# Optimization experiments

Measured on AMD Instinct MI355X. Metric: run time of the kernel, lower is better.

Reference implementation:

```python
import jax, jax.numpy as jnp
import numpy as np
from jax import lax

B, CIN, IMG = 32, 3, 128   # batch, image channels, image size
D, K = 256, 512            # codebook dim, codebook size


def _conv(x, w, stride, pad):
    # PyTorch Conv2d (bias=False), NCHW / OIHW
    return lax.conv_general_dilated(x, w, (stride, stride), ((pad, pad), (pad, pad)),
                                    dimension_numbers=('NCHW', 'OIHW', 'NCHW'))


def _deconv(x, w, b):
    # PyTorch ConvTranspose2d(k=4, s=2, p=1): lhs_dilation=2, pad=k-1-p=2, flipped kernel,
    # weight layout (in, out, kh, kw) -> 'IOHW'
    y = lax.conv_general_dilated(x, jnp.flip(w, (2, 3)), (1, 1), ((2, 2), (2, 2)),
                                 lhs_dilation=(2, 2),
                                 dimension_numbers=('NCHW', 'IOHW', 'NCHW'))
    return y + b[None, :, None, None]


def _res(x, w1, w2):
    # Faithful to the source ResidualBlock: relu1 output is DISCARDED (conv1 applied to x)
    out = _conv(x, w1, 1, 1)      # 3x3, pad 1
    out = jax.nn.relu(out)
    out = _conv(out, w2, 1, 0)    # 1x1, pad 0
    return out + x


def setup_inputs() -> dict:
    key = jax.random.key(0)
    ks = jax.random.split(key, 20)
    s = 0.05
    inp = {
        'x': jax.random.uniform(ks[0], (B, CIN, IMG, IMG), jnp.float32),
        # codebook, init uniform(-1/K, 1/K) as in init_weights
        'embed_w': jax.random.uniform(ks[1], (K, D), jnp.float32, -1.0 / K, 1.0 / K),
        # encoder
        'e_w1': jax.random.normal(ks[2], (D, CIN, 4, 4), jnp.float32) * s,
        'e_w2': jax.random.normal(ks[3], (D, D, 4, 4), jnp.float32) * s,
        'e_r1a': jax.random.normal(ks[4], (D, D, 3, 3), jnp.float32) * s,
        'e_r1b': jax.random.normal(ks[5], (D, D, 1, 1), jnp.float32) * s,
        'e_r2a': jax.random.normal(ks[6], (D, D, 3, 3), jnp.float32) * s,
        'e_r2b': jax.random.normal(ks[7], (D, D, 1, 1), jnp.float32) * s,
        # decoder
        'd_r1a': jax.random.normal(ks[8], (D, D, 3, 3), jnp.float32) * s,
        'd_r1b': jax.random.normal(ks[9], (D, D, 1, 1), jnp.float32) * s,
        'd_r2a': jax.random.normal(ks[10], (D, D, 3, 3), jnp.float32) * s,
        'd_r2b': jax.random.normal(ks[11], (D, D, 1, 1), jnp.float32) * s,
        'dt1_w': jax.random.normal(ks[12], (D, D, 4, 4), jnp.float32) * s,  # (in,out,kh,kw)
        'dt1_b': jnp.zeros((D,), jnp.float32),
        'dt2_w': jax.random.normal(ks[13], (D, CIN, 4, 4), jnp.float32) * s,
        'dt2_b': jnp.zeros((CIN,), jnp.float32),
    }
    return inp


def reference(x, embed_w, e_w1, e_w2, e_r1a, e_r1b, e_r2a, e_r2b,
              d_r1a, d_r1b, d_r2a, d_r2b, dt1_w, dt1_b, dt2_w, dt2_b):
    # ---- encoder (BN layers exist but are never called in the source forward) ----
    h = jax.nn.relu(_conv(x, e_w1, 2, 1))          # (B,D,64,64)
    h = jax.nn.relu(_conv(h, e_w2, 2, 1))          # (B,D,32,32)
    h = _res(h, e_r1a, e_r1b)
    z_e = _res(h, e_r2a, e_r2b)                    # (B,D,H,W)

    # ---- vector quantisation ----
    ze = jnp.transpose(z_e, (0, 2, 3, 1))          # (B,H,W,D)
    # squared L2 distances via expansion (same argmin/values as the broadcast diff tensor)
    d2 = (jnp.sum(ze * ze, -1, keepdims=True)      # (B,H,W,1)
          - 2.0 * jnp.einsum('bhwd,kd->bhwk', ze, embed_w)
          + jnp.sum(embed_w * embed_w, -1))        # (B,H,W,K)
    dist = jnp.sqrt(jnp.maximum(d2, 0.0))          # torch.norm(p=2) before min
    idx = jnp.argmin(dist, axis=-1)                # (B,H,W)
    z_q = embed_w[idx]                             # (B,H,W,D) gather

    # losses: source averages over an extra duplicated K axis, identical to mean over B,H,W
    sg = lax.stop_gradient
    loss1 = jnp.mean(jnp.sum((ze - sg(z_q)) ** 2, -1))   # grads -> encoder
    loss2 = jnp.mean(jnp.sum((sg(ze) - z_q) ** 2, -1))   # grads -> codebook

    # ---- decoder (takes z_q; BN layers never called; relu after deconv1 only) ----
    dq = jnp.transpose(z_q, (0, 3, 1, 2))          # (B,D,H,W)
    dq = _res(dq, d_r1a, d_r1b)
    dq = _res(dq, d_r2a, d_r2b)
    dq = jax.nn.relu(_deconv(dq, dt1_w, dt1_b))    # (B,D,64,64)
    recon = jax.nn.sigmoid(_deconv(dq, dt2_w, dt2_b))  # (B,3,128,128)
    return recon, loss1, loss2
```

## Files before the change

### kernel.cpp

```cpp
#include <hip/hip_runtime.h>


typedef __attribute__((ext_vector_type(8))) short bf16x8;
typedef __attribute__((ext_vector_type(4))) float f32x4;
#define MFMA_B16(a, b, c) __builtin_amdgcn_mfma_f32_16x16x32_bf16(a, b, c, 0, 0, 0)

__device__ inline unsigned short f2b(float f) {
    unsigned int u = __float_as_uint(f);
    unsigned int r = u + 0x7fffu + ((u >> 16) & 1u);
    return (unsigned short)(r >> 16);
}
__device__ inline float b2f(unsigned short u) {
    return __uint_as_float(((unsigned int)u) << 16);
}

struct PermfArgs {
    const float* src[10];
    int kw[10];
    int so[10], si[10], sh[10], sw[10];
    int cum[11];
};

__global__ void prep_all_k(PermfArgs a, unsigned short* __restrict__ dst,
                           const float* __restrict__ dt2_w, unsigned short* __restrict__ wg,
                           const float* __restrict__ embed, unsigned short* __restrict__ embF,
                           const float* __restrict__ e_w1, unsigned short* __restrict__ wgc,
                           float* __restrict__ nrm, float* __restrict__ lacc)
{
    int blkid = blockIdx.x;
    int tid = threadIdx.x;
    if (blkid < 18432) {
        int gid = blkid * 256 + tid;
        if (gid >= a.cum[10]) return;
        int seg = 0;
        while (seg < 9 && gid >= a.cum[seg + 1]) ++seg;
        int l = gid - a.cum[seg];
        int q = l & 31;
        int n = (l >> 5) & 255;
        int rest = l >> 13;
        int cch = rest & 7;
        int khkw = rest >> 3;
        int kh = khkw / a.kw[seg], kw = khkw % a.kw[seg];
        int ci = cch * 32 + q;
        dst[gid] = f2b(a.src[seg][n * a.so[seg] + ci * a.si[seg] + kh * a.sh[seg] + kw * a.sw[seg]]);
        return;
    }
    int blk = blkid - 18432;
    if (blk < 48) {
        int idx = blk * 256 + tid;
        int q = idx & 31;
        int n = (idx >> 5) % 48;
        int cch = idx / (48 * 32);
        int ci = cch * 32 + q;
        int oc = n % 3, khkw = n / 3;
        int kh = khkw >> 2, kw = khkw & 3;
        wg[idx] = f2b(dt2_w[ci * 48 + oc * 16 + kh * 4 + kw]);
    } else if (blk < 560) {
        int idx = (blk - 48) * 256 + tid;
        int q = idx & 31;
        int n = (idx >> 5) & 511;
        int cch = idx >> 14;
        embF[idx] = f2b(embed[n * 256 + cch * 32 + q]);
    } else if (blk < 624) {
        int idx = (blk - 560) * 256 + tid;
        int q = idx & 31;
        int n = (idx >> 5) & 255;
        int kt = idx >> 13;
        int k = kt * 32 + q;
        float v = 0.f;
        if (k < 48) {
            int ci = k >> 4, kh = (k >> 2) & 3, kwv = k & 3;
            v = e_w1[n * 48 + ci * 16 + kh * 4 + kwv];
        }
        wgc[idx] = f2b(v);
    } else if (blk < 752) {
        int row = (blk - 624) * 4 + (tid >> 6);
        int lane = tid & 63;
        float s = 0.f;
        #pragma unroll
        for (int c = 0; c < 256; c += 64) {
            float v = embed[row * 256 + c + lane];
            s += v * v;
        }
        #pragma unroll
        for (int off = 1; off < 64; off <<= 1) s += __shfl_xor(s, off);
        if (lane == 0) nrm[row] = s;
    } else {
        if (tid == 0) lacc[0] = 0.f;
    }
}

__global__ void __launch_bounds__(256, 4)
conv1m_k(const float* __restrict__ x, const unsigned short* __restrict__ wgc,
         unsigned short* __restrict__ out)
{
    int bh = blockIdx.x;
    int b = bh >> 6, oh = bh & 63;
    int tid = threadIdx.x;
    int lane = tid & 63, wv = tid >> 6;
    int m = lane & 15, quad = lane >> 4;
    __shared__ float xrow[3][4][130];
    __shared__ __align__(16) unsigned short imc[64 * 72];
    __shared__ __align__(16) unsigned short obuf[32 * 264];
    for (int s = tid; s < 1560; s += 256) {
        int col = s % 130;
        int t = s / 130;
        int r = t & 3;
        int c = t >> 2;
        int ih = 2 * oh - 1 + r, iw = col - 1;
        float v = 0.f;
        if ((unsigned)ih < 128u && (unsigned)iw < 128u)
            v = x[(((b * 3 + c) << 7) + ih) * 128 + iw];
        xrow[c][r][col] = v;
    }
    __syncthreads();
    for (int s = tid; s < 4096; s += 256) {
        int px = s >> 6, k = s & 63;
        float v = 0.f;
        if (k < 48) {
            int ci = k >> 4, kh = (k >> 2) & 3, kw = k & 3;
            v = xrow[ci][kh][2 * px + kw];
        }
        imc[px * 72 + k] = f2b(v);
    }
    __syncthreads();
    f32x4 acc[16];
    f32x4 z = {0.f, 0.f, 0.f, 0.f};
    #pragma unroll
    for (int i = 0; i < 16; ++i) acc[i] = z;
    bf16x8 a0 = *(const bf16x8*)&imc[((wv << 4) + m) * 72 + (quad << 3)];
    bf16x8 a1 = *(const bf16x8*)&imc[((wv << 4) + m) * 72 + 32 + (quad << 3)];
    #pragma unroll
    for (int nt = 0; nt < 16; ++nt) {
        bf16x8 b0 = *(const bf16x8*)&wgc[(nt * 16 + m) * 32 + (quad << 3)];
        bf16x8 b1 = *(const bf16x8*)&wgc[(256 + nt * 16 + m) * 32 + (quad << 3)];
        acc[nt] = MFMA_B16(a0, b0, acc[nt]);
        acc[nt] = MFMA_B16(a1, b1, acc[nt]);
    }
    for (int h = 0; h < 2; ++h) {
        __syncthreads();
        if ((wv >> 1) == h) {
            #pragma unroll
            for (int nt = 0; nt < 16; ++nt)
                #pragma unroll
                for (int r = 0; r < 4; ++r) {
                    int pxl = ((wv & 1) << 4) + quad * 4 + r;
                    obuf[pxl * 264 + nt * 16 + m] = f2b(fmaxf(acc[nt][r], 0.f));
                }
        }
        __syncthreads();
        int pxl2 = tid >> 3, seg = tid & 7;
        int gp = (bh << 6) + 32 * h + pxl2;
        #pragma unroll
        for (int u = 0; u < 4; ++u)
            *(int4*)&out[(gp << 8) + seg * 32 + u * 8] = *(int4*)&obuf[pxl2 * 264 + seg * 32 + u * 8];
    }
}

__global__ void __launch_bounds__(256, 4)
mconv2_k(const unsigned short* __restrict__ in, const unsigned short* __restrict__ wf,
         unsigned short* __restrict__ out)
{
    int blk = blockIdx.x;
    int bb = blk >> 5;
    int rem = blk & 31;
    int j = rem >> 1;
    int nh = rem & 1;
    int tid = threadIdx.x;
    int lane = tid & 63;
    int wv = tid >> 6;
    int n0 = (nh << 7) + (wv << 5);
    int m = lane & 15, quad = lane >> 4;
    __shared__ __align__(16) unsigned short win[2 * 66 * 132];
    f32x4 acc[2][2][2];
    f32x4 z = {0.f, 0.f, 0.f, 0.f};
    #pragma unroll
    for (int a = 0; a < 2; ++a)
        #pragma unroll
        for (int i = 0; i < 2; ++i)
            #pragma unroll
            for (int t = 0; t < 2; ++t) acc[a][i][t] = z;

    for (int c0 = 0; c0 < 256; c0 += 128) {
        for (int kh = 0; kh < 4; ++kh) {
            __syncthreads();
            for (int s = tid; s < 2 * 66 * 16; s += 256) {
                int c16 = s & 15;
                int t2 = s >> 4;
                int col = t2 % 66;
                int rr = t2 / 66;
                int ih = 4 * j - 1 + kh + 2 * rr, iw = col - 1;
                int4 v = make_int4(0, 0, 0, 0);
                if ((unsigned)ih < 64u && (unsigned)iw < 64u)
                    v = *(const int4*)&in[((((bb << 6) + ih) << 6) + iw) * 256 + c0 + (c16 << 3)];
                int cs = (col >> 1) + (col & 1) * 33;
                *(int4*)&win[(rr * 66 + cs) * 132 + (c16 << 3)] = v;
            }
            __syncthreads();
            #pragma unroll
            for (int kw = 0; kw < 4; ++kw) {
                int csoff = (kw >> 1) + (kw & 1) * 33;
                #pragma unroll
                for (int cch = 0; cch < 4; ++cch) {
                    bf16x8 a00 = *(const bf16x8*)&win[(m + csoff) * 132 + (cch << 5) + (quad << 3)];
                    bf16x8 a01 = *(const bf16x8*)&win[(m + 16 + csoff) * 132 + (cch << 5) + (quad << 3)];
                    bf16x8 a10 = *(const bf16x8*)&win[(66 + m + csoff) * 132 + (cch << 5) + (quad << 3)];
                    bf16x8 a11 = *(const bf16x8*)&win[(66 + m + 16 + csoff) * 132 + (cch << 5) + (quad << 3)];
                    int cg = (c0 >> 5) + cch;
                    int wbase = ((((kh << 2) + kw) * 8 + cg) * 256 + n0 + m) * 32 + (quad << 3);
                    bf16x8 b0 = *(const bf16x8*)&wf[wbase];
                    bf16x8 b1 = *(const bf16x8*)&wf[wbase + 16 * 32];
                    acc[0][0][0] = MFMA_B16(a00, b0, acc[0][0][0]);
                    acc[0][0][1] = MFMA_B16(a00, b1, acc[0][0][1]);
                    acc[0][1][0] = MFMA_B16(a01, b0, acc[0][1][0]);
                    acc[0][1][1] = MFMA_B16(a01, b1, acc[0][1][1]);
                    acc[1][0][0] = MFMA_B16(a10, b0, acc[1][0][0]);
                    acc[1][0][1] = MFMA_B16(a10, b1, acc[1][0][1]);
                    acc[1][1][0] = MFMA_B16(a11, b0, acc[1][1][0]);
                    acc[1][1][1] = MFMA_B16(a11, b1, acc[1][1][1]);
                }
            }
        }
    }
    for (int row = 0; row < 2; ++row) {
        __syncthreads();
        #pragma unroll
        for (int mt = 0; mt < 2; ++mt)
            #pragma unroll
            for (int nt = 0; nt < 2; ++nt)
                #pragma unroll
                for (int r = 0; r < 4; ++r) {
                    int px = mt * 16 + quad * 4 + r;
                    int lcol = (wv << 5) + nt * 16 + m;
                    win[px * 136 + lcol] = f2b(fmaxf(acc[row][mt][nt][r], 0.f));
                }
        __syncthreads();
        int oh = 2 * j + row;
        int px2 = tid >> 3, seg = tid & 7;
        int gb = ((((bb << 5) + oh) << 5) + px2) * 256 + (nh << 7) + seg * 16;
        *(int4*)&out[gb]     = *(int4*)&win[px2 * 136 + seg * 16];
        *(int4*)&out[gb + 8] = *(int4*)&win[px2 * 136 + seg * 16 + 8];
    }
}

__global__ void __launch_bounds__(256, 4)
mres_k(const unsigned short* __restrict__ in, const unsigned short* __restrict__ wf3,
       const unsigned short* __restrict__ wf1, const unsigned short* __restrict__ res,
       unsigned short* __restrict__ outb, float* __restrict__ outf, int f32out)
{
    int blk = blockIdx.x;
    int bb = blk >> 5, oh = blk & 31;
    int tid = threadIdx.x;
    int lane = tid & 63;
    int n0 = (tid >> 6) << 6;
    int m = lane & 15, quad = lane >> 4;
    __shared__ __align__(16) unsigned short win[3 * 34 * 132];
    f32x4 acc[2][4];
    f32x4 z = {0.f, 0.f, 0.f, 0.f};
    #pragma unroll
    for (int i = 0; i < 2; ++i)
        #pragma unroll
        for (int t = 0; t < 4; ++t) acc[i][t] = z;

    for (int c0 = 0; c0 < 256; c0 += 128) {
        __syncthreads();
        for (int s = tid; s < 3 * 34 * 16; s += 256) {
            int c16 = s & 15;
            int t2 = s >> 4;
            int col = t2 % 34;
            int rr = t2 / 34;
            int ih = oh - 1 + rr, iw = col - 1;
            int4 v = make_int4(0, 0, 0, 0);
            if ((unsigned)ih < 32u && (unsigned)iw < 32u)
                v = *(const int4*)&in[((((bb << 5) + ih) << 5) + iw) * 256 + c0 + (c16 << 3)];
            *(int4*)&win[(rr * 34 + col) * 132 + (c16 << 3)] = v;
        }
        __syncthreads();
        for (int kh = 0; kh < 3; ++kh) {
            #pragma unroll
            for (int kw = 0; kw < 3; ++kw) {
                #pragma unroll
                for (int cch = 0; cch < 4; ++cch) {
                    const unsigned short* ba = &win[(kh * 34 + m + kw) * 132 + (cch << 5) + (quad << 3)];
                    bf16x8 a0 = *(const bf16x8*)ba;
                    bf16x8 a1 = *(const bf16x8*)(ba + 16 * 132);
                    int cg = (c0 >> 5) + cch;
                    int wbase = (((kh * 3 + kw) * 8 + cg) * 256 + n0 + m) * 32 + (quad << 3);
                    bf16x8 b0 = *(const bf16x8*)&wf3[wbase];
                    bf16x8 b1 = *(const bf16x8*)&wf3[wbase + 16 * 32];
                    bf16x8 b2 = *(const bf16x8*)&wf3[wbase + 32 * 32];
                    bf16x8 b3 = *(const bf16x8*)&wf3[wbase + 48 * 32];
                    acc[0][0] = MFMA_B16(a0, b0, acc[0][0]);
                    acc[0][1] = MFMA_B16(a0, b1, acc[0][1]);
                    acc[0][2] = MFMA_B16(a0, b2, acc[0][2]);
                    acc[0][3] = MFMA_B16(a0, b3, acc[0][3]);
                    acc[1][0] = MFMA_B16(a1, b0, acc[1][0]);
                    acc[1][1] = MFMA_B16(a1, b1, acc[1][1]);
                    acc[1][2] = MFMA_B16(a1, b2, acc[1][2]);
                    acc[1][3] = MFMA_B16(a1, b3, acc[1][3]);
                }
            }
        }
    }

    __syncthreads();
    unsigned short* mid = win;
    #pragma unroll
    for (int mt = 0; mt < 2; ++mt)
        #pragma unroll
        for (int nt = 0; nt < 4; ++nt)
            #pragma unroll
            for (int r = 0; r < 4; ++r) {
                int px = mt * 16 + quad * 4 + r;
                int col = n0 + nt * 16 + m;
                mid[px * 264 + col] = f2b(fmaxf(acc[mt][nt][r], 0.f));
            }
    __syncthreads();

    f32x4 acc2[2][4];
    #pragma unroll
    for (int i = 0; i < 2; ++i)
        #pragma unroll
        for (int t = 0; t < 4; ++t) acc2[i][t] = z;
    #pragma unroll
    for (int cch = 0; cch < 8; ++cch) {
        bf16x8 a0 = *(const bf16x8*)&mid[m * 264 + (cch << 5) + (quad << 3)];
        bf16x8 a1 = *(const bf16x8*)&mid[(m + 16) * 264 + (cch << 5) + (quad << 3)];
        int wbase = (cch * 256 + n0 + m) * 32 + (quad << 3);
        bf16x8 b0 = *(const bf16x8*)&wf1[wbase];
        bf16x8 b1 = *(const bf16x8*)&wf1[wbase + 16 * 32];
        bf16x8 b2 = *(const bf16x8*)&wf1[wbase + 32 * 32];
        bf16x8 b3 = *(const bf16x8*)&wf1[wbase + 48 * 32];
        acc2[0][0] = MFMA_B16(a0, b0, acc2[0][0]);
        acc2[0][1] = MFMA_B16(a0, b1, acc2[0][1]);
        acc2[0][2] = MFMA_B16(a0, b2, acc2[0][2]);
        acc2[0][3] = MFMA_B16(a0, b3, acc2[0][3]);
        acc2[1][0] = MFMA_B16(a1, b0, acc2[1][0]);
        acc2[1][1] = MFMA_B16(a1, b1, acc2[1][1]);
        acc2[1][2] = MFMA_B16(a1, b2, acc2[1][2]);
        acc2[1][3] = MFMA_B16(a1, b3, acc2[1][3]);
    }
    __syncthreads();
    #pragma unroll
    for (int mt = 0; mt < 2; ++mt)
        #pragma unroll
        for (int nt = 0; nt < 4; ++nt)
            #pragma unroll
            for (int r = 0; r < 4; ++r) {
                int px = mt * 16 + quad * 4 + r;
                int col = n0 + nt * 16 + m;
                mid[px * 264 + col] = f2b(acc2[mt][nt][r]);
            }
    __syncthreads();
    int rowbase = blk << 13;
    int px2 = tid >> 3, seg = tid & 7;
    #pragma unroll
    for (int u = 0; u < 4; ++u) {
        int c0 = seg * 32 + u * 8;
        int gb = rowbase + (px2 << 8) + c0;
        int4 av4 = *(const int4*)&mid[px2 * 264 + c0];
        int4 rv4 = *(const int4*)&res[gb];
        const unsigned short* ap = (const unsigned short*)&av4;
        const unsigned short* rp = (const unsigned short*)&rv4;
        float v[8];
        unsigned short ob[8];
        #pragma unroll
        for (int j2 = 0; j2 < 8; ++j2) {
            v[j2] = b2f(ap[j2]) + b2f(rp[j2]);
            ob[j2] = f2b(v[j2]);
        }
        *(int4*)&outb[gb] = *(int4*)ob;
        if (f32out) {
            *(float4*)&outf[gb] = make_float4(v[0], v[1], v[2], v[3]);
            *(float4*)&outf[gb + 4] = make_float4(v[4], v[5], v[6], v[7]);
        }
    }
}

__global__ void __launch_bounds__(256, 4)
mdeconv1_k(const unsigned short* __restrict__ in, const unsigned short* __restrict__ wf,
           const float* __restrict__ bias, unsigned short* __restrict__ out)
{
    int blk = blockIdx.x;
    int bb = blk >> 5;
    int rem = blk & 31;
    int pp = rem >> 4;
    int i = rem & 15;
    int oy_a = pp + 4 * i;
    int p = (oy_a + 1) & 1;
    int r0a = (oy_a + 1 - p) >> 1;
    int rbase = r0a - 1;
    int tid = threadIdx.x;
    int lane = tid & 63;
    int n0 = (tid >> 6) << 6;
    int m = lane & 15, quad = lane >> 4;
    __shared__ __align__(16) unsigned short win[3 * 34 * 132];

    for (int par = 0; par < 2; ++par) {
        f32x4 acc[2][2][4];
        f32x4 z = {0.f, 0.f, 0.f, 0.f};
        #pragma unroll
        for (int a = 0; a < 2; ++a)
            #pragma unroll
            for (int i2 = 0; i2 < 2; ++i2)
                #pragma unroll
                for (int t = 0; t < 4; ++t) acc[a][i2][t] = z;

        for (int c0 = 0; c0 < 256; c0 += 128) {
            __syncthreads();
            for (int s = tid; s < 3 * 34 * 16; s += 256) {
                int c16 = s & 15;
                int t2 = s >> 4;
                int col = t2 % 34;
                int rr = t2 / 34;
                int ih = rbase + rr, iw = col - 1;
                int4 v = make_int4(0, 0, 0, 0);
                if ((unsigned)ih < 32u && (unsigned)iw < 32u)
                    v = *(const int4*)&in[((((bb << 5) + ih) << 5) + iw) * 256 + c0 + (c16 << 3)];
                *(int4*)&win[(rr * 34 + col) * 132 + (c16 << 3)] = v;
            }
            __syncthreads();
            #pragma unroll
            for (int t = 0; t < 2; ++t) {
                int kh = p + 2 * t;
                #pragma unroll
                for (int u = 0; u < 2; ++u) {
                    int kw = (1 - par) + 2 * u;
                    int ixoff = par - u + 1;
                    #pragma unroll
                    for (int cch = 0; cch < 4; ++cch) {
                        const unsigned short* baA = &win[((1 - t) * 34 + m + ixoff) * 132 + (cch << 5) + (quad << 3)];
                        const unsigned short* baB = &win[((2 - t) * 34 + m + ixoff) * 132 + (cch << 5) + (quad << 3)];
                        bf16x8 a00 = *(const bf16x8*)baA;
                        bf16x8 a01 = *(const bf16x8*)(baA + 16 * 132);
                        bf16x8 a10 = *(const bf16x8*)baB;
                        bf16x8 a11 = *(const bf16x8*)(baB + 16 * 132);
                        int cg = (c0 >> 5) + cch;
                        int wbase = ((((kh << 2) + kw) * 8 + cg) * 256 + n0 + m) * 32 + (quad << 3);
                        bf16x8 b0 = *(const bf16x8*)&wf[wbase];
                        bf16x8 b1 = *(const bf16x8*)&wf[wbase + 16 * 32];
                        bf16x8 b2 = *(const bf16x8*)&wf[wbase + 32 * 32];
                        bf16x8 b3 = *(const bf16x8*)&wf[wbase + 48 * 32];
                        acc[0][0][0] = MFMA_B16(a00, b0, acc[0][0][0]);
                        acc[0][0][1] = MFMA_B16(a00, b1, acc[0][0][1]);
                        acc[0][0][2] = MFMA_B16(a00, b2, acc[0][0][2]);
                        acc[0][0][3] = MFMA_B16(a00, b3, acc[0][0][3]);
                        acc[0][1][0] = MFMA_B16(a01, b0, acc[0][1][0]);
                        acc[0][1][1] = MFMA_B16(a01, b1, acc[0][1][1]);
                        acc[0][1][2] = MFMA_B16(a01, b2, acc[0][1][2]);
                        acc[0][1][3] = MFMA_B16(a01, b3, acc[0][1][3]);
                        acc[1][0][0] = MFMA_B16(a10, b0, acc[1][0][0]);
                        acc[1][0][1] = MFMA_B16(a10, b1, acc[1][0][1]);
                        acc[1][0][2] = MFMA_B16(a10, b2, acc[1][0][2]);
                        acc[1][0][3] = MFMA_B16(a10, b3, acc[1][0][3]);
                        acc[1][1][0] = MFMA_B16(a11, b0, acc[1][1][0]);
                        acc[1][1][1] = MFMA_B16(a11, b1, acc[1][1][1]);
                        acc[1][1][2] = MFMA_B16(a11, b2, acc[1][1][2]);
                        acc[1][1][3] = MFMA_B16(a11, b3, acc[1][1][3]);
                    }
                }
            }
        }
        #pragma unroll
        for (int row = 0; row < 2; ++row) {
            int oy = oy_a + 2 * row;
            __syncthreads();
            #pragma unroll
            for (int mt = 0; mt < 2; ++mt)
                #pragma unroll
                for (int nt = 0; nt < 4; ++nt) {
                    int col = n0 + nt * 16 + m;
                    float bs = bias[col];
                    #pragma unroll
                    for (int r = 0; r < 4; ++r) {
                        int oxi = mt * 16 + quad * 4 + r;
                        win[oxi * 264 + col] = f2b(fmaxf(acc[row][mt][nt][r] + bs, 0.f));
                    }
                }
            __syncthreads();
            int oxi2 = tid >> 3, seg = tid & 7;
            int gb = ((((bb << 6) + oy) << 6) + 2 * oxi2 + par) * 256 + seg * 32;
            #pragma unroll
            for (int u = 0; u < 4; ++u)
                *(int4*)&out[gb + u * 8] = *(int4*)&win[oxi2 * 264 + seg * 32 + u * 8];
        }
    }
}

__global__ void __launch_bounds__(256, 2)
vqm_k(const unsigned short* __restrict__ zeb, const float* __restrict__ zef,
      const unsigned short* __restrict__ embF, const float* __restrict__ embed,
      const float* __restrict__ nrm, unsigned short* __restrict__ zq,
      float* __restrict__ lacc)
{
    int bh = blockIdx.x;
    int tid = threadIdx.x;
    int lane = tid & 63;
    int wv = tid >> 6;
    int m = lane & 15, quad = lane >> 4;
    __shared__ __align__(16) unsigned short win[32 * 264];
    __shared__ float bvv[4][32];
    __shared__ int   bii[4][32];
    __shared__ int   bidx[32];
    int rowbase = bh << 13;
    for (int s = tid; s < 32 * 32; s += 256) {
        int c8 = s & 31, px = s >> 5;
        *(int4*)&win[px * 264 + (c8 << 3)] = *(const int4*)&zeb[rowbase + (px << 8) + (c8 << 3)];
    }
    __syncthreads();

    f32x4 acc[2][8];
    f32x4 z = {0.f, 0.f, 0.f, 0.f};
    #pragma unroll
    for (int i = 0; i < 2; ++i)
        #pragma unroll
        for (int j = 0; j < 8; ++j) acc[i][j] = z;

    #pragma unroll
    for (int cch = 0; cch < 8; ++cch) {
        bf16x8 a0 = *(const bf16x8*)&win[m * 264 + (cch << 5) + (quad << 3)];
        bf16x8 a1 = *(const bf16x8*)&win[(m + 16) * 264 + (cch << 5) + (quad << 3)];
        #pragma unroll
        for (int nt = 0; nt < 8; ++nt) {
            bf16x8 b = *(const bf16x8*)&embF[((cch << 9) + (wv << 7) + (nt << 4) + m) * 32 + (quad << 3)];
            acc[0][nt] = MFMA_B16(a0, b, acc[0][nt]);
            acc[1][nt] = MFMA_B16(a1, b, acc[1][nt]);
        }
    }

    float nv[8];
    #pragma unroll
    for (int nt = 0; nt < 8; ++nt) nv[nt] = nrm[(wv << 7) + (nt << 4) + m];

    #pragma unroll
    for (int mt = 0; mt < 2; ++mt)
        #pragma unroll
        for (int r = 0; r < 4; ++r) {
            float bv = 1e30f;
            int bi = 0x7fffffff;
            #pragma unroll
            for (int nt = 0; nt < 8; ++nt) {
                float d = nv[nt] - 2.f * acc[mt][nt][r];
                int n = (wv << 7) + (nt << 4) + m;
                if (d < bv || (d == bv && n < bi)) { bv = d; bi = n; }
            }
            #pragma unroll
            for (int off = 1; off < 16; off <<= 1) {
                float ov = __shfl_xor(bv, off);
                int oi = __shfl_xor(bi, off);
                if (ov < bv || (ov == bv && oi < bi)) { bv = ov; bi = oi; }
            }
            if (m == 0) {
                int px = mt * 16 + quad * 4 + r;
                bvv[wv][px] = bv;
                bii[wv][px] = bi;
            }
        }
    __syncthreads();
    if (tid < 32) {
        float bv = bvv[0][tid];
        int bi = bii[0][tid];
        #pragma unroll
        for (int w2 = 1; w2 < 4; ++w2) {
            float ov = bvv[w2][tid];
            int oi = bii[w2][tid];
            if (ov < bv || (ov == bv && oi < bi)) { bv = ov; bi = oi; }
        }
        bidx[tid] = bi;
    }
    __syncthreads();

    float lsum = 0.f;
    #pragma unroll
    for (int j = 0; j < 8; ++j) {
        int px = (wv << 3) + j;
        int bi = bidx[px];
        int pix = (bh << 5) + px;
        const float4 e = *(const float4*)&embed[bi * 256 + (lane << 2)];
        const float4 zv = *(const float4*)&zef[(pix << 8) + (lane << 2)];
        ushort4 eq;
        eq.x = f2b(e.x); eq.y = f2b(e.y); eq.z = f2b(e.z); eq.w = f2b(e.w);
        *(ushort4*)&zq[(pix << 8) + (lane << 2)] = eq;
        float dx = zv.x - e.x, dy = zv.y - e.y, dz = zv.z - e.z, dw = zv.w - e.w;
        lsum += dx * dx + dy * dy + dz * dz + dw * dw;
    }
    #pragma unroll
    for (int off = 1; off < 64; off <<= 1) lsum += __shfl_xor(lsum, off);
    if (lane == 0) atomicAdd(lacc, lsum);
}

__global__ void __launch_bounds__(256, 4)
mdec2a_k(const unsigned short* __restrict__ in, const unsigned short* __restrict__ wg,
         float* __restrict__ Y)
{
    int tid = threadIdx.x;
    int lane = tid & 63;
    int wv = tid >> 6;
    int m = lane & 15, quad = lane >> 4;
    __shared__ __align__(16) unsigned short win[64 * 264];
    int pxbase = blockIdx.x << 6;
    for (int s = tid; s < 64 * 32; s += 256) {
        int c8 = s & 31, px = s >> 5;
        *(int4*)&win[px * 264 + (c8 << 3)] = *(const int4*)&in[((pxbase + px) << 8) + (c8 << 3)];
    }
    __syncthreads();
    f32x4 acc[3];
    f32x4 z = {0.f, 0.f, 0.f, 0.f};
    acc[0] = z; acc[1] = z; acc[2] = z;
    #pragma unroll
    for (int cch = 0; cch < 8; ++cch) {
        bf16x8 a = *(const bf16x8*)&win[((wv << 4) + m) * 264 + (cch << 5) + (quad << 3)];
        #pragma unroll
        for (int nt = 0; nt < 3; ++nt) {
            bf16x8 b = *(const bf16x8*)&wg[(cch * 48 + nt * 16 + m) * 32 + (quad << 3)];
            acc[nt] = MFMA_B16(a, b, acc[nt]);
        }
    }
    #pragma unroll
    for (int nt = 0; nt < 3; ++nt)
        #pragma unroll
        for (int r = 0; r < 4; ++r) {
            int px = pxbase + (wv << 4) + quad * 4 + r;
            Y[px * 48 + nt * 16 + m] = acc[nt][r];
        }
}

__global__ void dec2b_k(const float* __restrict__ Y, const float* __restrict__ bias,
                        const float* __restrict__ lacc, float* __restrict__ out)
{
    if (blockIdx.x == 0 && threadIdx.x == 0) {
        float mloss = lacc[0] * (1.0f / 32768.0f);
        out[1572864] = mloss;
        out[1572865] = mloss;
    }
    int idx = blockIdx.x * 256 + threadIdx.x;
    int b = idx >> 14;
    int rem = idx & 16383;
    int oy = rem >> 7;
    int ox = rem & 127;
    int p = (oy + 1) & 1;
    int q = (ox + 1) & 1;
    float acc0 = bias[0], acc1 = bias[1], acc2 = bias[2];
    #pragma unroll
    for (int t = 0; t < 2; ++t) {
        int kh = p + 2 * t;
        int ih = (oy + 1 - kh) >> 1;
        if ((unsigned)ih >= 64u) continue;
        #pragma unroll
        for (int u = 0; u < 2; ++u) {
            int kw = q + 2 * u;
            int iw = (ox + 1 - kw) >> 1;
            if ((unsigned)iw >= 64u) continue;
            int base = ((((b << 6) + ih) << 6) + iw) * 48 + ((kh << 2) + kw) * 3;
            acc0 += Y[base];
            acc1 += Y[base + 1];
            acc2 += Y[base + 2];
        }
    }
    int obase = (b * 3 << 14) + (oy << 7) + ox;
    out[obase]           = 1.f / (1.f + expf(-acc0));
    out[obase + 16384]   = 1.f / (1.f + expf(-acc1));
    out[obase + 32768]   = 1.f / (1.f + expf(-acc2));
}

extern "C" void kernel_launch(void* const* d_in, const int* in_sizes, int n_in,
                              void* d_out, int out_size, void* d_ws, size_t ws_size,
                              hipStream_t stream)
{
    (void)in_sizes; (void)n_in; (void)out_size; (void)ws_size;
    const float* x      = (const float*)d_in[0];
    const float* embed  = (const float*)d_in[1];
    const float* e_w1   = (const float*)d_in[2];
    const float* e_w2   = (const float*)d_in[3];
    const float* e_r1a  = (const float*)d_in[4];
    const float* e_r1b  = (const float*)d_in[5];
    const float* e_r2a  = (const float*)d_in[6];
    const float* e_r2b  = (const float*)d_in[7];
    const float* d_r1a  = (const float*)d_in[8];
    const float* d_r1b  = (const float*)d_in[9];
    const float* d_r2a  = (const float*)d_in[10];
    const float* d_r2b  = (const float*)d_in[11];
    const float* dt1_w  = (const float*)d_in[12];
    const float* dt1_b  = (const float*)d_in[13];
    const float* dt2_w  = (const float*)d_in[14];
    const float* dt2_b  = (const float*)d_in[15];
    float* outp = (float*)d_out;

    char* base = (char*)d_ws;
    size_t off = 0;
    auto alloc = [&](size_t bytes) { char* p = base + off; off += (bytes + 255) & ~size_t(255); return p; };
    unsigned short* A0b = (unsigned short*)alloc(67108864);
    float*          A1f = (float*)alloc(33554432);
    unsigned short* L0  = (unsigned short*)alloc(16777216);
    unsigned short* L1  = (unsigned short*)alloc(16777216);
    unsigned short* Wf  = (unsigned short*)alloc(9437184);
    unsigned short* Wg  = (unsigned short*)alloc(24576);
    unsigned short* EmbF = (unsigned short*)alloc(262144);
    unsigned short* WgC = (unsigned short*)alloc(32768);
    float* Nrm  = (float*)alloc(2048);
    float* Lacc = (float*)alloc(64);
    float* Y = A1f;

    unsigned short* Wf_ew2  = Wf;
    unsigned short* Wf_er1a = Wf + 1048576;
    unsigned short* Wf_er1b = Wf + 1638400;
    unsigned short* Wf_er2a = Wf + 1703936;
    unsigned short* Wf_er2b = Wf + 2293760;
    unsigned short* Wf_dr1a = Wf + 2359296;
    unsigned short* Wf_dr1b = Wf + 2949120;
    unsigned short* Wf_dr2a = Wf + 3014656;
    unsigned short* Wf_dr2b = Wf + 3604480;
    unsigned short* Wf_dt1  = Wf + 3670016;

    PermfArgs pa;
    const float* srcs[10] = {e_w2, e_r1a, e_r1b, e_r2a, e_r2b, d_r1a, d_r1b, d_r2a, d_r2b, dt1_w};
    int kws[10] = {4, 3, 1, 3, 1, 3, 1, 3, 1, 4};
    int sos[10] = {4096, 2304, 256, 2304, 256, 2304, 256, 2304, 256, 16};
    int sis[10] = {16, 9, 1, 9, 1, 9, 1, 9, 1, 4096};
    int shs[10] = {4, 3, 0, 3, 0, 3, 0, 3, 0, 4};
    int sws[10] = {1, 1, 0, 1, 0, 1, 0, 1, 0, 1};
    int cums[11] = {0, 1048576, 1638400, 1703936, 2293760, 2359296,
                    2949120, 3014656, 3604480, 3670016, 4718592};
    for (int k = 0; k < 10; ++k) {
        pa.src[k] = srcs[k]; pa.kw[k] = kws[k]; pa.so[k] = sos[k];
        pa.si[k] = sis[k]; pa.sh[k] = shs[k]; pa.sw[k] = sws[k];
        pa.cum[k] = cums[k];
    }
    pa.cum[10] = cums[10];

    prep_all_k<<<19185, 256, 0, stream>>>(pa, Wf, dt2_w, Wg, embed, EmbF, e_w1, WgC, Nrm, Lacc);

    conv1m_k<<<32 * 64, 256, 0, stream>>>(x, WgC, A0b);
    mconv2_k<<<32 * 32, 256, 0, stream>>>(A0b, Wf_ew2, L1);
    mres_k<<<32 * 32, 256, 0, stream>>>(L1, Wf_er1a, Wf_er1b, L1, L0, nullptr, 0);
    mres_k<<<32 * 32, 256, 0, stream>>>(L0, Wf_er2a, Wf_er2b, L0, L1, A1f, 1);

    vqm_k<<<32 * 32, 256, 0, stream>>>(L1, A1f, EmbF, embed, Nrm, L1, Lacc);

    mres_k<<<32 * 32, 256, 0, stream>>>(L1, Wf_dr1a, Wf_dr1b, L1, L0, nullptr, 0);
    mres_k<<<32 * 32, 256, 0, stream>>>(L0, Wf_dr2a, Wf_dr2b, L0, L1, nullptr, 0);
    mdeconv1_k<<<32 * 32, 256, 0, stream>>>(L1, Wf_dt1, dt1_b, A0b);
    mdec2a_k<<<2048, 256, 0, stream>>>(A0b, Wg, Y);
    dec2b_k<<<2048, 256, 0, stream>>>(Y, dt2_b, Lacc, outp);
}
```

Baseline: 856.2 us.

## Stage full channel depth in LDS for res and deconv1, one output row per block

The residual conv kernel now loads all 256 input channels of its 3-row window into LDS at once instead of two 128-channel halves, removing a barrier/reload phase. The first deconvolution kernel is restructured so each block computes one output row (both column parities) from a 2-row full-channel window, doubling the grid and writing a contiguous 64-pixel row with coalesced stores. The change trades larger LDS footprints and lower occupancy bounds for fewer synchronisations and simpler staging, and deconv1 loses the previous sharing of weight loads across two output rows.

```diff
diff --git a/kernel.cpp b/kernel.cpp
--- a/kernel.cpp
+++ b/kernel.cpp
@@ -243,7 +243,7 @@
     }
 }
 
-__global__ void __launch_bounds__(256, 4)
+__global__ void __launch_bounds__(256, 2)
 mres_k(const unsigned short* __restrict__ in, const unsigned short* __restrict__ wf3,
        const unsigned short* __restrict__ wf1, const unsigned short* __restrict__ res,
        unsigned short* __restrict__ outb, float* __restrict__ outf, int f32out)
@@ -254,7 +254,7 @@
     int lane = tid & 63;
     int n0 = (tid >> 6) << 6;
     int m = lane & 15, quad = lane >> 4;
-    __shared__ __align__(16) unsigned short win[3 * 34 * 132];
+    __shared__ __align__(16) unsigned short win[3 * 34 * 264];
     f32x4 acc[2][4];
     f32x4 z = {0.f, 0.f, 0.f, 0.f};
     #pragma unroll
@@ -262,43 +262,40 @@
         #pragma unroll
         for (int t = 0; t < 4; ++t) acc[i][t] = z;
 
-    for (int c0 = 0; c0 < 256; c0 += 128) {
-        __syncthreads();
-        for (int s = tid; s < 3 * 34 * 16; s += 256) {
-            int c16 = s & 15;
-            int t2 = s >> 4;
-            int col = t2 % 34;
-            int rr = t2 / 34;
-            int ih = oh - 1 + rr, iw = col - 1;
-            int4 v = make_int4(0, 0, 0, 0);
-            if ((unsigned)ih < 32u && (unsigned)iw < 32u)
-                v = *(const int4*)&in[((((bb << 5) + ih) << 5) + iw) * 256 + c0 + (c16 << 3)];
-            *(int4*)&win[(rr * 34 + col) * 132 + (c16 << 3)] = v;
-        }
-        __syncthreads();
-        for (int kh = 0; kh < 3; ++kh) {
-            #pragma unroll
-            for (int kw = 0; kw < 3; ++kw) {
-                #pragma unroll
-                for (int cch = 0; cch < 4; ++cch) {
-                    const unsigned short* ba = &win[(kh * 34 + m + kw) * 132 + (cch << 5) + (quad << 3)];
-                    bf16x8 a0 = *(const bf16x8*)ba;
-                    bf16x8 a1 = *(const bf16x8*)(ba + 16 * 132);
-                    int cg = (c0 >> 5) + cch;
-                    int wbase = (((kh * 3 + kw) * 8 + cg) * 256 + n0 + m) * 32 + (quad << 3);
-                    bf16x8 b0 = *(const bf16x8*)&wf3[wbase];
-                    bf16x8 b1 = *(const bf16x8*)&wf3[wbase + 16 * 32];
-                    bf16x8 b2 = *(const bf16x8*)&wf3[wbase + 32 * 32];
-                    bf16x8 b3 = *(const bf16x8*)&wf3[wbase + 48 * 32];
-                    acc[0][0] = MFMA_B16(a0, b0, acc[0][0]);
-                    acc[0][1] = MFMA_B16(a0, b1, acc[0][1]);
-                    acc[0][2] = MFMA_B16(a0, b2, acc[0][2]);
-                    acc[0][3] = MFMA_B16(a0, b3, acc[0][3]);
-                    acc[1][0] = MFMA_B16(a1, b0, acc[1][0]);
-                    acc[1][1] = MFMA_B16(a1, b1, acc[1][1]);
-                    acc[1][2] = MFMA_B16(a1, b2, acc[1][2]);
-                    acc[1][3] = MFMA_B16(a1, b3, acc[1][3]);
-                }
+    for (int s = tid; s < 3 * 34 * 32; s += 256) {
+        int c8 = s & 31;
+        int t2 = s >> 5;
+        int col = t2 % 34;
+        int rr = t2 / 34;
+        int ih = oh - 1 + rr, iw = col - 1;
+        int4 v = make_int4(0, 0, 0, 0);
+        if ((unsigned)ih < 32u && (unsigned)iw < 32u)
+            v = *(const int4*)&in[((((bb << 5) + ih) << 5) + iw) * 256 + (c8 << 3)];
+        *(int4*)&win[(rr * 34 + col) * 264 + (c8 << 3)] = v;
+    }
+    __syncthreads();
+
+    for (int kh = 0; kh < 3; ++kh) {
+        #pragma unroll
+        for (int kw = 0; kw < 3; ++kw) {
+            #pragma unroll
+            for (int cch = 0; cch < 8; ++cch) {
+                const unsigned short* ba = &win[(kh * 34 + m + kw) * 264 + (cch << 5) + (quad << 3)];
+                bf16x8 a0 = *(const bf16x8*)ba;
+                bf16x8 a1 = *(const bf16x8*)(ba + 16 * 264);
+                int wbase = (((kh * 3 + kw) * 8 + cch) * 256 + n0 + m) * 32 + (quad << 3);
+                bf16x8 b0 = *(const bf16x8*)&wf3[wbase];
+                bf16x8 b1 = *(const bf16x8*)&wf3[wbase + 16 * 32];
+                bf16x8 b2 = *(const bf16x8*)&wf3[wbase + 32 * 32];
+                bf16x8 b3 = *(const bf16x8*)&wf3[wbase + 48 * 32];
+                acc[0][0] = MFMA_B16(a0, b0, acc[0][0]);
+                acc[0][1] = MFMA_B16(a0, b1, acc[0][1]);
+                acc[0][2] = MFMA_B16(a0, b2, acc[0][2]);
+                acc[0][3] = MFMA_B16(a0, b3, acc[0][3]);
+                acc[1][0] = MFMA_B16(a1, b0, acc[1][0]);
+                acc[1][1] = MFMA_B16(a1, b1, acc[1][1]);
+                acc[1][2] = MFMA_B16(a1, b2, acc[1][2]);
+                acc[1][3] = MFMA_B16(a1, b3, acc[1][3]);
             }
         }
     }
@@ -377,113 +374,94 @@
     }
 }
 
-__global__ void __launch_bounds__(256, 4)
+__global__ void __launch_bounds__(256, 3)
 mdeconv1_k(const unsigned short* __restrict__ in, const unsigned short* __restrict__ wf,
            const float* __restrict__ bias, unsigned short* __restrict__ out)
 {
     int blk = blockIdx.x;
-    int bb = blk >> 5;
-    int rem = blk & 31;
-    int pp = rem >> 4;
-    int i = rem & 15;
-    int oy_a = pp + 4 * i;
-    int p = (oy_a + 1) & 1;
-    int r0a = (oy_a + 1 - p) >> 1;
-    int rbase = r0a - 1;
+    int bb = blk >> 6, oy = blk & 63;
+    int p = (oy + 1) & 1;
+    int r0 = (oy + 1 - p) >> 1;
     int tid = threadIdx.x;
     int lane = tid & 63;
     int n0 = (tid >> 6) << 6;
     int m = lane & 15, quad = lane >> 4;
-    __shared__ __align__(16) unsigned short win[3 * 34 * 132];
-
+    __shared__ __align__(16) unsigned short win[2 * 34 * 264];
+
+    for (int s = tid; s < 2 * 34 * 32; s += 256) {
+        int c8 = s & 31;
+        int t2 = s >> 5;
+        int col = t2 % 34;
+        int t = t2 / 34;
+        int ih = r0 - t, iw = col - 1;
+        int4 v = make_int4(0, 0, 0, 0);
+        if ((unsigned)ih < 32u && (unsigned)iw < 32u)
+            v = *(const int4*)&in[((((bb << 5) + ih) << 5) + iw) * 256 + (c8 << 3)];
+        *(int4*)&win[(t * 34 + col) * 264 + (c8 << 3)] = v;
+    }
+    __syncthreads();
+
+    f32x4 acc[2][2][4];
+    f32x4 z = {0.f, 0.f, 0.f, 0.f};
+    #pragma unroll
+    for (int a = 0; a < 2; ++a)
+        #pragma unroll
+        for (int i2 = 0; i2 < 2; ++i2)
+            #pragma unroll
+            for (int t = 0; t < 4; ++t) acc[a][i2][t] = z;
+
+    #pragma unroll
     for (int par = 0; par < 2; ++par) {
-        f32x4 acc[2][2][4];
-        f32x4 z = {0.f, 0.f, 0.f, 0.f};
-        #pragma unroll
-        for (int a = 0; a < 2; ++a)
-            #pragma unroll
-            for (int i2 = 0; i2 < 2; ++i2)
+        #pragma unroll
+        for (int t = 0; t < 2; ++t) {
+            int kh = p + 2 * t;
+            #pragma unroll
+            for (int u = 0; u < 2; ++u) {
+                int kw = (1 - par) + 2 * u;
+                int ixoff = par - u + 1;
                 #pragma unroll
-                for (int t = 0; t < 4; ++t) acc[a][i2][t] = z;
-
-        for (int c0 = 0; c0 < 256; c0 += 128) {
-            __syncthreads();
-            for (int s = tid; s < 3 * 34 * 16; s += 256) {
-                int c16 = s & 15;
-                int t2 = s >> 4;
-                int col = t2 % 34;
-                int rr = t2 / 34;
-                int ih = rbase + rr, iw = col - 1;
-                int4 v = make_int4(0, 0, 0, 0);
-                if ((unsigned)ih < 32u && (unsigned)iw < 32u)
-                    v = *(const int4*)&in[((((bb << 5) + ih) << 5) + iw) * 256 + c0 + (c16 << 3)];
-                *(int4*)&win[(rr * 34 + col) * 132 + (c16 << 3)] = v;
-            }
-            __syncthreads();
-            #pragma unroll
-            for (int t = 0; t < 2; ++t) {
-                int kh = p + 2 * t;
+                for (int cch = 0; cch < 8; ++cch) {
+                    const unsigned short* ba = &win[(t * 34 + m + ixoff) * 264 + (cch << 5) + (quad << 3)];
+                    bf16x8 a0 = *(const bf16x8*)ba;
+                    bf16x8 a1 = *(const bf16x8*)(ba + 16 * 264);
+                    int wbase = ((((kh << 2) + kw) * 8 + cch) * 256 + n0 + m) * 32 + (quad << 3);
+                    bf16x8 b0 = *(const bf16x8*)&wf[wbase];
+                    bf16x8 b1 = *(const bf16x8*)&wf[wbase + 16 * 32];
+                    bf16x8 b2 = *(const bf16x8*)&wf[wbase + 32 * 32];
+                    bf16x8 b3 = *(const bf16x8*)&wf[wbase + 48 * 32];
+                    acc[par][0][0] = MFMA_B16(a0, b0, acc[par][0][0]);
+                    acc[par][0][1] = MFMA_B16(a0, b1, acc[par][0][1]);
+                    acc[par][0][2] = MFMA_B16(a0, b2, acc[par][0][2]);
+                    acc[par][0][3] = MFMA_B16(a0, b3, acc[par][0][3]);
+                    acc[par][1][0] = MFMA_B16(a1, b0, acc[par][1][0]);
+                    acc[par][1][1] = MFMA_B16(a1, b1, acc[par][1][1]);
+                    acc[par][1][2] = MFMA_B16(a1, b2, acc[par][1][2]);
+                    acc[par][1][3] = MFMA_B16(a1, b3, acc[par][1][3]);
+                }
+            }
+        }
+    }
+
+    __syncthreads();
+    #pragma unroll
+    for (int par = 0; par < 2; ++par)
+        #pragma unroll
+        for (int mt = 0; mt < 2; ++mt)
+            #pragma unroll
+            for (int nt = 0; nt < 4; ++nt) {
+                int col = n0 + nt * 16 + m;
+                float bs = bias[col];
                 #pragma unroll
-                for (int u = 0; u < 2; ++u) {
-                    int kw = (1 - par) + 2 * u;
-                    int ixoff = par - u + 1;
-                    #pragma unroll
-                    for (int cch = 0; cch < 4; ++cch) {
-                        const unsigned short* baA = &win[((1 - t) * 34 + m + ixoff) * 132 + (cch << 5) + (quad << 3)];
-                        const unsigned short* baB = &win[((2 - t) * 34 + m + ixoff) * 132 + (cch << 5) + (quad << 3)];
-                        bf16x8 a00 = *(const bf16x8*)baA;
-                        bf16x8 a01 = *(const bf16x8*)(baA + 16 * 132);
-                        bf16x8 a10 = *(const bf16x8*)baB;
-                        bf16x8 a11 = *(const bf16x8*)(baB + 16 * 132);
-                        int cg = (c0 >> 5) + cch;
-                        int wbase = ((((kh << 2) + kw) * 8 + cg) * 256 + n0 + m) * 32 + (quad << 3);
-                        bf16x8 b0 = *(const bf16x8*)&wf[wbase];
-                        bf16x8 b1 = *(const bf16x8*)&wf[wbase + 16 * 32];
-                        bf16x8 b2 = *(const bf16x8*)&wf[wbase + 32 * 32];
-                        bf16x8 b3 = *(const bf16x8*)&wf[wbase + 48 * 32];
-                        acc[0][0][0] = MFMA_B16(a00, b0, acc[0][0][0]);
-                        acc[0][0][1] = MFMA_B16(a00, b1, acc[0][0][1]);
-                        acc[0][0][2] = MFMA_B16(a00, b2, acc[0][0][2]);
-                        acc[0][0][3] = MFMA_B16(a00, b3, acc[0][0][3]);
-                        acc[0][1][0] = MFMA_B16(a01, b0, acc[0][1][0]);
-                        acc[0][1][1] = MFMA_B16(a01, b1, acc[0][1][1]);
-                        acc[0][1][2] = MFMA_B16(a01, b2, acc[0][1][2]);
-                        acc[0][1][3] = MFMA_B16(a01, b3, acc[0][1][3]);
-                        acc[1][0][0] = MFMA_B16(a10, b0, acc[1][0][0]);
-                        acc[1][0][1] = MFMA_B16(a10, b1, acc[1][0][1]);
-                        acc[1][0][2] = MFMA_B16(a10, b2, acc[1][0][2]);
-                        acc[1][0][3] = MFMA_B16(a10, b3, acc[1][0][3]);
-                        acc[1][1][0] = MFMA_B16(a11, b0, acc[1][1][0]);
-                        acc[1][1][1] = MFMA_B16(a11, b1, acc[1][1][1]);
-                        acc[1][1][2] = MFMA_B16(a11, b2, acc[1][1][2]);
-                        acc[1][1][3] = MFMA_B16(a11, b3, acc[1][1][3]);
-                    }
+                for (int r = 0; r < 4; ++r) {
+                    int ox = 2 * (mt * 16 + quad * 4 + r) + par;
+                    win[ox * 264 + col] = f2b(fmaxf(acc[par][mt][nt][r] + bs, 0.f));
                 }
             }
-        }
-        #pragma unroll
-        for (int row = 0; row < 2; ++row) {
-            int oy = oy_a + 2 * row;
-            __syncthreads();
-            #pragma unroll
-            for (int mt = 0; mt < 2; ++mt)
-                #pragma unroll
-                for (int nt = 0; nt < 4; ++nt) {
-                    int col = n0 + nt * 16 + m;
-                    float bs = bias[col];
-                    #pragma unroll
-                    for (int r = 0; r < 4; ++r) {
-                        int oxi = mt * 16 + quad * 4 + r;
-                        win[oxi * 264 + col] = f2b(fmaxf(acc[row][mt][nt][r] + bs, 0.f));
-                    }
-                }
-            __syncthreads();
-            int oxi2 = tid >> 3, seg = tid & 7;
-            int gb = ((((bb << 6) + oy) << 6) + 2 * oxi2 + par) * 256 + seg * 32;
-            #pragma unroll
-            for (int u = 0; u < 4; ++u)
-                *(int4*)&out[gb + u * 8] = *(int4*)&win[oxi2 * 264 + seg * 32 + u * 8];
-        }
+    __syncthreads();
+    int rowbase = ((bb << 6) + oy) << 6;
+    for (int s = tid; s < 64 * 32; s += 256) {
+        int c8 = s & 31, px = s >> 5;
+        *(int4*)&out[((rowbase + px) << 8) + (c8 << 3)] = *(int4*)&win[px * 264 + (c8 << 3)];
     }
 }
 
@@ -739,7 +717,7 @@
 
     mres_k<<<32 * 32, 256, 0, stream>>>(L1, Wf_dr1a, Wf_dr1b, L1, L0, nullptr, 0);
     mres_k<<<32 * 32, 256, 0, stream>>>(L0, Wf_dr2a, Wf_dr2b, L0, L1, nullptr, 0);
-    mdeconv1_k<<<32 * 32, 256, 0, stream>>>(L1, Wf_dt1, dt1_b, A0b);
+    mdeconv1_k<<<32 * 64, 256, 0, stream>>>(L1, Wf_dt1, dt1_b, A0b);
     mdec2a_k<<<2048, 256, 0, stream>>>(A0b, Wg, Y);
     dec2b_k<<<2048, 256, 0, stream>>>(Y, dt2_b, Lacc, outp);
 }
```

Result: slower. 917.9 us (+7.2%).
